# Kernel tuning notes

Measured on AMD Instinct MI355X. Metric: run time of the kernel, lower is better.

The kernel has to match this reference:

```python
import jax, jax.numpy as jnp
import numpy as np

OUT_H, OUT_W = 7, 7
SPATIAL_SCALE = 0.0625
N_IMG, C, H, W = 2, 256, 38, 38
NUM_ROIS = 256
IMG_MAX = 607.9  # keeps floor(coord*scale) <= 37


def setup_inputs() -> dict:
    key = jax.random.key(0)
    k_feat, k_b, k_xa, k_xb, k_ya, k_yb = jax.random.split(key, 6)
    feat = jax.random.normal(k_feat, (N_IMG, C, H, W), dtype=jnp.float32)
    bidx = jax.random.randint(k_b, (NUM_ROIS,), 0, N_IMG).astype(jnp.float32)
    xa = jax.random.uniform(k_xa, (NUM_ROIS,), minval=0.0, maxval=IMG_MAX)
    xb = jax.random.uniform(k_xb, (NUM_ROIS,), minval=0.0, maxval=IMG_MAX)
    ya = jax.random.uniform(k_ya, (NUM_ROIS,), minval=0.0, maxval=IMG_MAX)
    yb = jax.random.uniform(k_yb, (NUM_ROIS,), minval=0.0, maxval=IMG_MAX)
    rois = jnp.stack([bidx,
                      jnp.minimum(xa, xb), jnp.minimum(ya, yb),
                      jnp.maximum(xa, xb), jnp.maximum(ya, yb)], axis=1)
    return {"input": feat, "rois": rois.astype(jnp.float32)}


def _roi_max_pool(feat_all, rois):
    # feat_all: (N, C, H, W); rois: (R, 5) = (batch_idx, x1, y1, x2, y2)
    H_, W_ = feat_all.shape[2], feat_all.shape[3]
    b = rois[:, 0].astype(jnp.int32)
    # torch: rois[:,1:].mul_(scale); rois.long() -> truncation (== floor for >=0)
    coords = jnp.floor(rois[:, 1:] * SPATIAL_SCALE).astype(jnp.int32)
    x1, y1, x2, y2 = coords[:, 0], coords[:, 1], coords[:, 2], coords[:, 3]
    rh = y2 - y1 + 1  # inclusive crop: [y1, y2+1)
    rw = x2 - x1 + 1
    feat = feat_all[b]  # (R, C, H, W) per-ROI gather of its image
    neg = jnp.array(-jnp.inf, feat.dtype)

    # separable adaptive max pool: rows then cols
    hs = jnp.arange(H_)
    rows = []
    for i in range(OUT_H):  # fixed small loop over output bins
        hstart = y1 + (i * rh) // OUT_H                       # floor(i*rh/OUT_H)
        hend = y1 + ((i + 1) * rh + OUT_H - 1) // OUT_H       # ceil
        m = (hs[None, :] >= hstart[:, None]) & (hs[None, :] < hend[:, None])  # (R,H)
        rows.append(jnp.max(jnp.where(m[:, None, :, None], feat, neg), axis=2))  # (R,C,W)
    rowmax = jnp.stack(rows, axis=2)  # (R, C, OUT_H, W)

    ws = jnp.arange(W_)
    cols = []
    for j in range(OUT_W):
        wstart = x1 + (j * rw) // OUT_W
        wend = x1 + ((j + 1) * rw + OUT_W - 1) // OUT_W
        m = (ws[None, :] >= wstart[:, None]) & (ws[None, :] < wend[:, None])  # (R,W)
        cols.append(jnp.max(jnp.where(m[:, None, None, :], rowmax, neg), axis=3))  # (R,C,OUT_H)
    return jnp.stack(cols, axis=3)  # (R, C, OUT_H, OUT_W)


def reference(input, rois):
    return _roi_max_pool(input, rois)
```

## Files before the change

### kernel.cpp

```cpp
#include <hip/hip_runtime.h>
#include <math.h>

#define OUT_H 7
#define OUT_W 7
#define N_C 256
#define FH 38
#define FW 38
#define NUM_ROIS 256
#define SPATIAL_SCALE 0.0625f
#define PLANE (FH * FW)

#define CC 16
#define CHUNKS (N_C / CC)

__global__ __launch_bounds__(266) void roi_pool_kernel(
    const float* __restrict__ feat,
    const float* __restrict__ rois,
    float* __restrict__ out)
{
    __shared__ float rowmax[CC][OUT_H][FW];
    __shared__ int wse[2][OUT_W];

    int blk   = blockIdx.x;
    int r     = blk / CHUNKS;
    int chunk = blk - r * CHUNKS;
    int c0    = chunk * CC;

    const float* roi = rois + r * 5;
    int b  = __builtin_amdgcn_readfirstlane((int)roi[0]);
    int x1 = __builtin_amdgcn_readfirstlane((int)(roi[1] * SPATIAL_SCALE));
    int y1 = __builtin_amdgcn_readfirstlane((int)(roi[2] * SPATIAL_SCALE));
    int x2 = __builtin_amdgcn_readfirstlane((int)(roi[3] * SPATIAL_SCALE));
    int y2 = __builtin_amdgcn_readfirstlane((int)(roi[4] * SPATIAL_SCALE));
    int rh = y2 - y1 + 1;
    int rw = x2 - x1 + 1;

    int tx = threadIdx.x;
    int ty = threadIdx.y;
    int tz = threadIdx.z;
    int lin = tx + 19 * (ty + 7 * tz);

    if (lin < OUT_W) {
        int j = lin;
        wse[0][j] = x1 + (j * rw) / OUT_W;
        wse[1][j] = x1 + ((j + 1) * rw + OUT_W - 1) / OUT_W;
    }

    int i = ty;
    int hstart = y1 + (i * rh) / OUT_H;
    int hend   = y1 + ((i + 1) * rh + OUT_H - 1) / OUT_H;

    const float* pbase = feat + ((size_t)b * N_C + c0 + tz * 8) * PLANE;
    int off = hstart * FW + 2 * tx;

    float2 m[8];
    #pragma unroll
    for (int cl = 0; cl < 8; ++cl) { m[cl].x = -INFINITY; m[cl].y = -INFINITY; }

    for (int h = hstart; h < hend; ++h, off += FW) {
        #pragma unroll
        for (int cl = 0; cl < 8; ++cl) {
            float2 v = *(const float2*)&pbase[cl * PLANE + off];
            m[cl].x = fmaxf(m[cl].x, v.x);
            m[cl].y = fmaxf(m[cl].y, v.y);
        }
    }

    #pragma unroll
    for (int cl = 0; cl < 8; ++cl)
        *(float2*)&rowmax[tz * 8 + cl][i][2 * tx] = m[cl];

    __syncthreads();

    if (lin < 196) {
        int g   = lin / 49;
        int pos = lin - g * 49;
        int oi  = pos / OUT_W;
        int j   = pos - oi * OUT_W;
        int wstart = wse[0][j];
        int wend   = wse[1][j];
        float* obase = out + ((size_t)r * N_C + c0) * (OUT_H * OUT_W);
        #pragma unroll
        for (int q = 0; q < 4; ++q) {
            int cl = g * 4 + q;
            float mm = -INFINITY;
            for (int ww = wstart; ww < wend; ++ww)
                mm = fmaxf(mm, rowmax[cl][oi][ww]);
            obase[cl * (OUT_H * OUT_W) + pos] = mm;
        }
    }
}

extern "C" void kernel_launch(void* const* d_in, const int* in_sizes, int n_in,
                              void* d_out, int out_size, void* d_ws, size_t ws_size,
                              hipStream_t stream) {
    const float* feat = (const float*)d_in[0];
    const float* rois = (const float*)d_in[1];
    float* out = (float*)d_out;

    dim3 block(19, OUT_H, 2);
    int  grid = NUM_ROIS * CHUNKS;
    roi_pool_kernel<<<grid, block, 0, stream>>>(feat, rois, out);
}
```

Before: 78.01 us.

## Stage ROI row band into LDS with float4 loads and shrink channel chunk

Each block now copies the ROI's row band (from y1 to y2, aligned to 4 floats) for 4 channels into shared memory using coalesced float4 loads. The row-max pass then reads from LDS instead of issuing strided float2 global loads, so each block handles 4 channels instead of 16 and the grid is four times larger. This is meant to improve global load efficiency and raise block-level parallelism. In exchange it adds an extra LDS round trip and a barrier, loads full rows even where the ROI is narrow, and uses a larger shared-memory footprint per block, which can limit occupancy.

```diff
diff --git a/kernel.cpp b/kernel.cpp
--- a/kernel.cpp
+++ b/kernel.cpp
@@ -6,18 +6,20 @@
 #define N_C 256
 #define FH 38
 #define FW 38
+#define PLANE (FH * FW)
 #define NUM_ROIS 256
 #define SPATIAL_SCALE 0.0625f
-#define PLANE (FH * FW)
 
-#define CC 16
+#define CC 4
 #define CHUNKS (N_C / CC)
+#define CH_STRIDE 1448
 
 __global__ __launch_bounds__(266) void roi_pool_kernel(
     const float* __restrict__ feat,
     const float* __restrict__ rois,
     float* __restrict__ out)
 {
+    __shared__ __align__(16) float chlds[CC][CH_STRIDE];
     __shared__ float rowmax[CC][OUT_H][FW];
     __shared__ int wse[2][OUT_W];
 
@@ -35,59 +37,60 @@
     int rh = y2 - y1 + 1;
     int rw = x2 - x1 + 1;
 
-    int tx = threadIdx.x;
-    int ty = threadIdx.y;
-    int tz = threadIdx.z;
+    int tx  = threadIdx.x;
+    int ty  = threadIdx.y;
+    int tz  = threadIdx.z;
     int lin = tx + 19 * (ty + 7 * tz);
 
     if (lin < OUT_W) {
-        int j = lin;
-        wse[0][j] = x1 + (j * rw) / OUT_W;
-        wse[1][j] = x1 + ((j + 1) * rw + OUT_W - 1) / OUT_W;
+        wse[0][lin] = x1 + (lin * rw) / OUT_W;
+        wse[1][lin] = x1 + ((lin + 1) * rw + OUT_W - 1) / OUT_W;
     }
+
+    int s0  = (y1 * FW) & ~3;
+    int s1  = (y2 + 1) * FW;
+    int nfl = (s1 - s0 + 3) & ~3;
+    int pm  = PLANE - s0;
+    if (nfl > pm) nfl = pm;
+    int nf4 = nfl >> 2;
+    const float* gbase = feat + ((size_t)b * N_C + c0) * PLANE + s0;
+    #pragma unroll
+    for (int cl = 0; cl < CC; ++cl) {
+        for (int k = lin; k < nf4; k += 266) {
+            float4 v = *(const float4*)(gbase + cl * PLANE + 4 * k);
+            *(float4*)&chlds[cl][4 * k] = v;
+        }
+    }
+    __syncthreads();
 
     int i = ty;
     int hstart = y1 + (i * rh) / OUT_H;
     int hend   = y1 + ((i + 1) * rh + OUT_H - 1) / OUT_H;
-
-    const float* pbase = feat + ((size_t)b * N_C + c0 + tz * 8) * PLANE;
-    int off = hstart * FW + 2 * tx;
-
-    float2 m[8];
-    #pragma unroll
-    for (int cl = 0; cl < 8; ++cl) { m[cl].x = -INFINITY; m[cl].y = -INFINITY; }
-
-    for (int h = hstart; h < hend; ++h, off += FW) {
-        #pragma unroll
-        for (int cl = 0; cl < 8; ++cl) {
-            float2 v = *(const float2*)&pbase[cl * PLANE + off];
-            m[cl].x = fmaxf(m[cl].x, v.x);
-            m[cl].y = fmaxf(m[cl].y, v.y);
-        }
+    int c2 = tz * 2;
+    float2 m0; m0.x = -INFINITY; m0.y = -INFINITY;
+    float2 m1 = m0;
+    int ofs = hstart * FW + 2 * tx - s0;
+    for (int h = hstart; h < hend; ++h, ofs += FW) {
+        float2 a  = *(const float2*)&chlds[c2 + 0][ofs];
+        float2 bb = *(const float2*)&chlds[c2 + 1][ofs];
+        m0.x = fmaxf(m0.x, a.x);   m0.y = fmaxf(m0.y, a.y);
+        m1.x = fmaxf(m1.x, bb.x);  m1.y = fmaxf(m1.y, bb.y);
     }
-
-    #pragma unroll
-    for (int cl = 0; cl < 8; ++cl)
-        *(float2*)&rowmax[tz * 8 + cl][i][2 * tx] = m[cl];
-
+    *(float2*)&rowmax[c2 + 0][i][2 * tx] = m0;
+    *(float2*)&rowmax[c2 + 1][i][2 * tx] = m1;
     __syncthreads();
 
-    if (lin < 196) {
-        int g   = lin / 49;
-        int pos = lin - g * 49;
+    if (lin < CC * OUT_H * OUT_W) {
+        int cl  = lin / 49;
+        int pos = lin - cl * 49;
         int oi  = pos / OUT_W;
         int j   = pos - oi * OUT_W;
-        int wstart = wse[0][j];
-        int wend   = wse[1][j];
-        float* obase = out + ((size_t)r * N_C + c0) * (OUT_H * OUT_W);
-        #pragma unroll
-        for (int q = 0; q < 4; ++q) {
-            int cl = g * 4 + q;
-            float mm = -INFINITY;
-            for (int ww = wstart; ww < wend; ++ww)
-                mm = fmaxf(mm, rowmax[cl][oi][ww]);
-            obase[cl * (OUT_H * OUT_W) + pos] = mm;
-        }
+        int ws  = wse[0][j];
+        int we  = wse[1][j];
+        float mm = -INFINITY;
+        for (int w = ws; w < we; ++w)
+            mm = fmaxf(mm, rowmax[cl][oi][w]);
+        out[((size_t)r * N_C + c0 + cl) * (OUT_H * OUT_W) + pos] = mm;
     }
 }
 
```

Result: slower. 93.06 us (+19.3%).
